# Kernel optimization log

Measured on AMD Instinct MI355X. Metric: run time of the kernel, lower is better.

The kernel has to match this reference:

```python
import jax, jax.numpy as jnp
import numpy as np

BIG = 1e9
EPS_BETA = 1e-6
EPS_BN = 1e-5

N_NODES = 50000
N_EDGES = 800000
IN_DIM = 128
OUT_DIM = 128


def setup_inputs() -> dict:
    key = jax.random.key(0)
    ks = jax.random.split(key, 8)
    h = jax.random.normal(ks[0], (N_NODES, IN_DIM), dtype=jnp.float32)
    src = jax.random.randint(ks[1], (N_EDGES,), 0, N_NODES, dtype=jnp.int32)
    dst = jax.random.randint(ks[2], (N_EDGES,), 0, N_NODES, dtype=jnp.int32)
    sigma_GD = jax.random.uniform(ks[3], (N_EDGES,), dtype=jnp.float32)
    fc_w = jax.random.normal(ks[4], (IN_DIM, OUT_DIM), dtype=jnp.float32) / np.sqrt(IN_DIM)
    fc_b = jax.random.normal(ks[5], (OUT_DIM,), dtype=jnp.float32) * 0.01
    attn_w = jax.random.normal(ks[6], (2 * OUT_DIM, 1), dtype=jnp.float32) / np.sqrt(2 * OUT_DIM)
    attn_b = jax.random.normal(ks[7], (1,), dtype=jnp.float32) * 0.01
    bn_gamma = jnp.ones((OUT_DIM,), dtype=jnp.float32)
    bn_beta = jnp.zeros((OUT_DIM,), dtype=jnp.float32)
    return {"h": h, "src": src, "dst": dst, "sigma_GD": sigma_GD,
            "fc_w": fc_w, "fc_b": fc_b, "attn_w": attn_w, "attn_b": attn_b,
            "bn_gamma": bn_gamma, "bn_beta": bn_beta}


def reference(h, src, dst, sigma_GD, fc_w, fc_b, attn_w, attn_b, bn_gamma, bn_beta):
    n = h.shape[0]
    # node projection
    z = h @ fc_w + fc_b                                   # [N, D]
    z = jnp.where(jnp.isinf(z), BIG, z)
    # per-edge attention logits: concat(src,dst) @ W == src@W1 + dst@W2 (avoid concat materialization)
    d = z.shape[1]
    w_src, w_dst = attn_w[:d], attn_w[d:]
    z_src = z[src]                                        # [E, D]
    a = z_src @ w_src + z[dst] @ w_dst + attn_b           # [E, 1]
    a = jnp.where(jnp.isinf(a), BIG, a)
    e = jax.nn.leaky_relu(a, negative_slope=0.01)[:, 0]   # [E]
    # segment softmax over incoming edges (mailbox softmax)
    m = jax.ops.segment_max(e, dst, num_segments=n)       # [N]
    ex = jnp.exp(e - m[dst])
    denom = jax.ops.segment_sum(ex, dst, num_segments=n)  # [N]
    alpha = ex / denom[dst]                               # [E]
    # beta: sigma_GD normalized per destination node
    bsum = jax.ops.segment_sum(sigma_GD, dst, num_segments=n)
    beta = sigma_GD / (bsum[dst] + EPS_BETA)              # [E]
    # weighted scatter-sum of source features
    h_new = jax.ops.segment_sum((alpha * beta)[:, None] * z_src, dst, num_segments=n)  # [N, D]
    h_new = jnp.where(jnp.isinf(h_new), BIG, h_new)
    # BatchNorm1d (training-mode batch stats, biased variance, as torch does)
    mu = h_new.mean(axis=0)
    var = ((h_new - mu) ** 2).mean(axis=0)
    h_bn = (h_new - mu) * jax.lax.rsqrt(var + EPS_BN) * bn_gamma + bn_beta
    return jax.nn.elu(h_bn)
```

## Files before the change

### kernel.cpp

```cpp
#include <hip/hip_runtime.h>
#include <hip/hip_fp16.h>
#include <math.h>

#define N_NODES 50000
#define N_EDGES 800000
#define BIGV 1000000000.0f
#define NBLK_SCAN 196
#define NBLK_GEMM 3125

typedef _Float16 half8 __attribute__((ext_vector_type(8)));
typedef float floatx4 __attribute__((ext_vector_type(4)));

__device__ __forceinline__ float clampinf(float x) { return isinf(x) ? BIGV : x; }

__global__ __launch_bounds__(256) void k_wcast(const float* __restrict__ W,
                                               __half* __restrict__ wt,
                                               int* __restrict__ cursor,
                                               float* __restrict__ bns)
{
    int idx = blockIdx.x * 256 + threadIdx.x;
    int n = idx >> 7, k = idx & 127;
    wt[idx] = __float2half(W[k * 128 + n]);
    for (int i = idx; i < N_NODES; i += 16384) cursor[i] = 0;
    if (idx < 256) bns[idx] = 0.f;
}

__global__ __launch_bounds__(256) void k_gemm(
    const float* __restrict__ h, const __half* __restrict__ wt,
    const float* __restrict__ bias, const float* __restrict__ attn_w,
    const int* __restrict__ dst, __half* __restrict__ zh,
    float* __restrict__ sv, float* __restrict__ tv,
    int* __restrict__ cursor, int* __restrict__ rank)
{
    __shared__ _Float16 hA[16][136];
    __shared__ float spart[4][16], tpart[4][16];

    const int tid = threadIdx.x;
    const int lane = tid & 63;
    const int wv = tid >> 6;
    const int l16 = lane & 15;
    const int oct = lane >> 4;
    const int n0 = wv << 5;
    const int node0 = blockIdx.x << 4;

    const int e = blockIdx.x * 256 + tid;
    const int d = dst[e];
    {
        const float4* h4 = (const float4*)(h + (size_t)node0 * 128);
        for (int i = tid; i < 512; i += 256) {
            int r = i >> 5, c4 = i & 31;
            float4 v = h4[i];
            union { __half2 h2[2]; uint2 u; } pk;
            pk.h2[0] = __floats2half2_rn(v.x, v.y);
            pk.h2[1] = __floats2half2_rn(v.z, v.w);
            *(uint2*)&hA[r][c4 << 2] = pk.u;
        }
    }
    rank[e] = atomicAdd(&cursor[d], 1);

    half8 bfrag[4][2];
    #pragma unroll
    for (int kk = 0; kk < 4; ++kk)
        #pragma unroll
        for (int t = 0; t < 2; ++t)
            bfrag[kk][t] = *(const half8*)(wt + (size_t)(n0 + t * 16 + l16) * 128
                                              + kk * 32 + oct * 8);

    const float bv0 = bias[n0 + l16],         bv1 = bias[n0 + 16 + l16];
    const float ws0 = attn_w[n0 + l16],       ws1 = attn_w[n0 + 16 + l16];
    const float wd0 = attn_w[128 + n0 + l16], wd1 = attn_w[128 + n0 + 16 + l16];

    __syncthreads();

    floatx4 acc0 = {0.f, 0.f, 0.f, 0.f};
    floatx4 acc1 = {0.f, 0.f, 0.f, 0.f};
    #pragma unroll
    for (int kk = 0; kk < 4; ++kk) {
        half8 a = *(const half8*)&hA[l16][(kk << 5) + (oct << 3)];
        acc0 = __builtin_amdgcn_mfma_f32_16x16x32_f16(a, bfrag[kk][0], acc0, 0, 0, 0);
        acc1 = __builtin_amdgcn_mfma_f32_16x16x32_f16(a, bfrag[kk][1], acc1, 0, 0, 0);
    }

    float s_acc[4], t_acc[4];
    #pragma unroll
    for (int r = 0; r < 4; ++r) {
        float z0 = clampinf(acc0[r] + bv0);
        float z1 = clampinf(acc1[r] + bv1);
        const int row = (oct << 2) + r;
        zh[(size_t)(node0 + row) * 128 + n0 + l16]      = __float2half(z0);
        zh[(size_t)(node0 + row) * 128 + n0 + 16 + l16] = __float2half(z1);
        s_acc[r] = z0 * ws0 + z1 * ws1;
        t_acc[r] = z0 * wd0 + z1 * wd1;
    }
    #pragma unroll
    for (int r = 0; r < 4; ++r) {
        #pragma unroll
        for (int o = 1; o < 16; o <<= 1) {
            s_acc[r] += __shfl_xor(s_acc[r], o);
            t_acc[r] += __shfl_xor(t_acc[r], o);
        }
    }
    if (l16 == 0) {
        #pragma unroll
        for (int r = 0; r < 4; ++r) {
            spart[wv][(oct << 2) + r] = s_acc[r];
            tpart[wv][(oct << 2) + r] = t_acc[r];
        }
    }
    __syncthreads();
    if (tid < 16) {
        sv[node0 + tid] = spart[0][tid] + spart[1][tid] + spart[2][tid] + spart[3][tid];
        tv[node0 + tid] = tpart[0][tid] + tpart[1][tid] + tpart[2][tid] + tpart[3][tid];
    }
}

__global__ __launch_bounds__(256) void k_scan_bsum(const int* __restrict__ cursor,
                                                   int* __restrict__ bsum)
{
    __shared__ int s[256];
    const int t = threadIdx.x;
    const int idx = blockIdx.x * 256 + t;
    s[t] = (idx < N_NODES) ? cursor[idx] : 0;
    __syncthreads();
    for (int off = 128; off; off >>= 1) {
        if (t < off) s[t] += s[t + off];
        __syncthreads();
    }
    if (t == 0) bsum[blockIdx.x] = s[0];
}

__global__ __launch_bounds__(256) void k_scan_final(const int* __restrict__ bsum,
                                                    const int* __restrict__ cursor_in,
                                                    int* __restrict__ colptr)
{
    __shared__ int rs[256];
    __shared__ int s[256];
    const int t = threadIdx.x;

    int rv = (t < NBLK_SCAN) ? bsum[t] : 0;
    rs[t] = rv;
    __syncthreads();
    for (int off = 1; off < 256; off <<= 1) {
        int u = (t >= off) ? rs[t - off] : 0;
        __syncthreads();
        rs[t] += u;
        __syncthreads();
    }
    const int broot = (blockIdx.x > 0) ? rs[blockIdx.x - 1] : 0;
    if (blockIdx.x == 0 && t == 255) colptr[N_NODES] = rs[255];

    const int idx = blockIdx.x * 256 + t;
    int v = (idx < N_NODES) ? cursor_in[idx] : 0;
    s[t] = v;
    __syncthreads();
    for (int off = 1; off < 256; off <<= 1) {
        int u = (t >= off) ? s[t - off] : 0;
        __syncthreads();
        s[t] += u;
        __syncthreads();
    }
    if (idx < N_NODES) colptr[idx] = broot + s[t] - v;
}

__global__ void k_scatter(const int* __restrict__ src, const int* __restrict__ dst,
                          const float* __restrict__ sigma,
                          const int* __restrict__ rank, const int* __restrict__ colptr,
                          const float* __restrict__ sv, const float* __restrict__ tv,
                          const float* __restrict__ attn_b,
                          float4* __restrict__ recs)
{
    int e = blockIdx.x * 256 + threadIdx.x;
    if (e < N_EDGES) {
        int s = src[e];
        int d = dst[e];
        float a = sv[s] + tv[d] + attn_b[0];
        a = clampinf(a);
        float ev = a > 0.f ? a : 0.01f * a;
        int pos = colptr[d] + rank[e];
        float4 rec;
        rec.x = __int_as_float(s);
        rec.y = sigma[e];
        rec.z = ev;
        rec.w = 0.f;
        recs[pos] = rec;
    }
}

__global__ __launch_bounds__(256) void k_agg(
    const int* __restrict__ colptr, const float4* __restrict__ recs,
    const __half* __restrict__ zh, float* __restrict__ out)
{
    const int lane = threadIdx.x & 63;
    const int node = blockIdx.x * 4 + (threadIdx.x >> 6);
    if (node >= N_NODES) return;
    const int base = colptr[node];
    const int deg = colptr[node + 1] - base;

    const int grp = lane >> 4;
    const int l16 = lane & 15;
    float acc[8] = {0.f, 0.f, 0.f, 0.f, 0.f, 0.f, 0.f, 0.f};

    if (deg > 0) {
        if (deg <= 64) {
            int sidx = 0; float sig = 0.f, e = -INFINITY;
            if (lane < deg) {
                float4 r = recs[base + lane];
                sidx = __float_as_int(r.x); sig = r.y; e = r.z;
            }
            float m = e;
            for (int o = 32; o; o >>= 1) m = fmaxf(m, __shfl_xor(m, o));
            float p = (lane < deg) ? __expf(e - m) : 0.f;
            float dn = p, bs = sig;
            for (int o = 32; o; o >>= 1) {
                dn += __shfl_xor(dn, o);
                bs += __shfl_xor(bs, o);
            }
            const float coef = p * sig * (1.0f / dn) / (bs + 1e-6f);
            for (int c = 0; c < deg; c += 4) {
                const int j = c + grp;
                const int js = (j < deg) ? j : 0;
                float cf = __shfl(coef, js);
                int sj = __shfl(sidx, js);
                if (j < deg) {
                    uint4 raw = *(const uint4*)(zh + ((size_t)sj << 7) + (l16 << 3));
                    const __half2* hp = (const __half2*)&raw;
                    #pragma unroll
                    for (int k = 0; k < 4; ++k) {
                        float2 f = __half22float2(hp[k]);
                        acc[2*k]   = fmaf(cf, f.x, acc[2*k]);
                        acc[2*k+1] = fmaf(cf, f.y, acc[2*k+1]);
                    }
                }
            }
        } else {
            float m = -INFINITY;
            for (int i = lane; i < deg; i += 64) m = fmaxf(m, recs[base + i].z);
            for (int o = 32; o; o >>= 1) m = fmaxf(m, __shfl_xor(m, o));
            float dn = 0.f, bs = 0.f;
            for (int i = lane; i < deg; i += 64) {
                float4 r = recs[base + i];
                dn += __expf(r.z - m); bs += r.y;
            }
            for (int o = 32; o; o >>= 1) {
                dn += __shfl_xor(dn, o);
                bs += __shfl_xor(bs, o);
            }
            const float scale = (1.0f / dn) / (bs + 1e-6f);
            for (int c = 0; c < deg; c += 64) {
                int i = c + lane;
                int sidx = 0; float coef = 0.f;
                if (i < deg) {
                    float4 r = recs[base + i];
                    sidx = __float_as_int(r.x);
                    coef = __expf(r.z - m) * r.y * scale;
                }
                const int cnt = min(64, deg - c);
                for (int j = 0; j < cnt; j += 4) {
                    const int jj = j + grp;
                    const int js = (jj < cnt) ? jj : 0;
                    float cf = __shfl(coef, js);
                    int sj = __shfl(sidx, js);
                    if (jj < cnt) {
                        uint4 raw = *(const uint4*)(zh + ((size_t)sj << 7) + (l16 << 3));
                        const __half2* hp = (const __half2*)&raw;
                        #pragma unroll
                        for (int k = 0; k < 4; ++k) {
                            float2 f = __half22float2(hp[k]);
                            acc[2*k]   = fmaf(cf, f.x, acc[2*k]);
                            acc[2*k+1] = fmaf(cf, f.y, acc[2*k+1]);
                        }
                    }
                }
            }
        }
    }
    #pragma unroll
    for (int k = 0; k < 8; ++k) {
        acc[k] += __shfl_xor(acc[k], 16);
        acc[k] += __shfl_xor(acc[k], 32);
    }
    if (grp == 0) {
        float4 o0, o1;
        o0.x = clampinf(acc[0]); o0.y = clampinf(acc[1]);
        o0.z = clampinf(acc[2]); o0.w = clampinf(acc[3]);
        o1.x = clampinf(acc[4]); o1.y = clampinf(acc[5]);
        o1.z = clampinf(acc[6]); o1.w = clampinf(acc[7]);
        float4* op = (float4*)(out + (size_t)node * 128 + (l16 << 3));
        op[0] = o0; op[1] = o1;
    }
}

__global__ __launch_bounds__(256) void k_bnstats(const float* __restrict__ hnew,
                                                 float* __restrict__ sums)
{
    const int f = threadIdx.x & 127;
    const int half_ = threadIdx.x >> 7;
    float s = 0.f, q = 0.f;
    for (int node = blockIdx.x * 2 + half_; node < N_NODES; node += gridDim.x * 2) {
        float v = hnew[(size_t)node * 128 + f];
        s += v;
        q += v * v;
    }
    __shared__ float ls[256], lq[256];
    ls[threadIdx.x] = s; lq[threadIdx.x] = q;
    __syncthreads();
    if (half_ == 0) {
        s += ls[threadIdx.x + 128];
        q += lq[threadIdx.x + 128];
        atomicAdd(&sums[f], s);
        atomicAdd(&sums[128 + f], q);
    }
}

__global__ __launch_bounds__(256) void k_bnapply(float* __restrict__ io,
                                                 const float* __restrict__ sums,
                                                 const float* __restrict__ gamma,
                                                 const float* __restrict__ beta)
{
    const size_t idx = (size_t)blockIdx.x * 256 + threadIdx.x;
    const int f = (int)(idx & 127);
    const float invn = 1.0f / (float)N_NODES;
    float mu = sums[f] * invn;
    float var = fmaxf(sums[128 + f] * invn - mu * mu, 0.f);
    float rs = rsqrtf(var + 1e-5f);
    float x = io[idx];
    float y = (x - mu) * rs * gamma[f] + beta[f];
    io[idx] = y > 0.f ? y : expm1f(y);
}

extern "C" void kernel_launch(void* const* d_in, const int* in_sizes, int n_in,
                              void* d_out, int out_size, void* d_ws, size_t ws_size,
                              hipStream_t stream)
{
    const float* h      = (const float*)d_in[0];
    const int*   src    = (const int*)  d_in[1];
    const int*   dst    = (const int*)  d_in[2];
    const float* sigma  = (const float*)d_in[3];
    const float* fc_w   = (const float*)d_in[4];
    const float* fc_b   = (const float*)d_in[5];
    const float* attn_w = (const float*)d_in[6];
    const float* attn_b = (const float*)d_in[7];
    const float* gamma  = (const float*)d_in[8];
    const float* beta   = (const float*)d_in[9];
    float* out = (float*)d_out;

    float4* recs   = (float4*)d_ws;
    __half* zh     = (__half*)(recs + N_EDGES);
    float*  sv     = (float*)(zh + (size_t)N_NODES * 128);
    float*  tv     = sv + N_NODES;
    float*  bns    = tv + N_NODES;
    int*    colptr = (int*)(bns + 256);
    int*    cursor = colptr + 50004;
    int*    bsum   = cursor + N_NODES;
    int*    broot  = bsum + 256;
    __half* wt     = (__half*)(broot + 256);
    int*    rank   = (int*)(wt + 128 * 128);

    k_wcast     <<<64, 256, 0, stream>>>(fc_w, wt, cursor, bns);
    k_gemm      <<<NBLK_GEMM, 256, 0, stream>>>(h, wt, fc_b, attn_w, dst,
                                                zh, sv, tv, cursor, rank);
    k_scan_bsum <<<NBLK_SCAN, 256, 0, stream>>>(cursor, bsum);
    k_scan_final<<<NBLK_SCAN, 256, 0, stream>>>(bsum, cursor, colptr);
    k_scatter   <<<N_EDGES / 256, 256, 0, stream>>>(src, dst, sigma, rank, colptr,
                                                    sv, tv, attn_b, recs);
    k_agg       <<<N_NODES / 4, 256, 0, stream>>>(colptr, recs, zh, out);
    k_bnstats   <<<256, 256, 0, stream>>>(out, bns);
    k_bnapply   <<<(N_NODES * 128) / 256, 256, 0, stream>>>(out, bns, gamma, beta);
}
```

Measured before the change: 235.4 us.

## Vectorize batchnorm kernels and defer rank atomic past LDS-only barriers in GEMM

```diff
diff --git a/kernel.cpp b/kernel.cpp
--- a/kernel.cpp
+++ b/kernel.cpp
@@ -12,6 +12,13 @@
 typedef float floatx4 __attribute__((ext_vector_type(4)));
 
 __device__ __forceinline__ float clampinf(float x) { return isinf(x) ? BIGV : x; }
+
+__device__ __forceinline__ void barrier_lgkm_only() {
+    __builtin_amdgcn_sched_barrier(0);
+    asm volatile("s_waitcnt lgkmcnt(0)" ::: "memory");
+    __builtin_amdgcn_s_barrier();
+    __builtin_amdgcn_sched_barrier(0);
+}
 
 __global__ __launch_bounds__(256) void k_wcast(const float* __restrict__ W,
                                                __half* __restrict__ wt,
@@ -45,6 +52,7 @@
 
     const int e = blockIdx.x * 256 + tid;
     const int d = dst[e];
+
     {
         const float4* h4 = (const float4*)(h + (size_t)node0 * 128);
         for (int i = tid; i < 512; i += 256) {
@@ -56,7 +64,6 @@
             *(uint2*)&hA[r][c4 << 2] = pk.u;
         }
     }
-    rank[e] = atomicAdd(&cursor[d], 1);
 
     half8 bfrag[4][2];
     #pragma unroll
@@ -70,7 +77,10 @@
     const float ws0 = attn_w[n0 + l16],       ws1 = attn_w[n0 + 16 + l16];
     const float wd0 = attn_w[128 + n0 + l16], wd1 = attn_w[128 + n0 + 16 + l16];
 
-    __syncthreads();
+    __builtin_amdgcn_sched_barrier(0);
+    const int rk = atomicAdd(&cursor[d], 1);
+
+    barrier_lgkm_only();
 
     floatx4 acc0 = {0.f, 0.f, 0.f, 0.f};
     floatx4 acc1 = {0.f, 0.f, 0.f, 0.f};
@@ -107,11 +117,12 @@
             tpart[wv][(oct << 2) + r] = t_acc[r];
         }
     }
-    __syncthreads();
+    barrier_lgkm_only();
     if (tid < 16) {
         sv[node0 + tid] = spart[0][tid] + spart[1][tid] + spart[2][tid] + spart[3][tid];
         tv[node0 + tid] = tpart[0][tid] + tpart[1][tid] + tpart[2][tid] + tpart[3][tid];
     }
+    rank[e] = rk;
 }
 
 __global__ __launch_bounds__(256) void k_scan_bsum(const int* __restrict__ cursor,
@@ -293,22 +304,36 @@
 __global__ __launch_bounds__(256) void k_bnstats(const float* __restrict__ hnew,
                                                  float* __restrict__ sums)
 {
-    const int f = threadIdx.x & 127;
-    const int half_ = threadIdx.x >> 7;
-    float s = 0.f, q = 0.f;
-    for (int node = blockIdx.x * 2 + half_; node < N_NODES; node += gridDim.x * 2) {
-        float v = hnew[(size_t)node * 128 + f];
-        s += v;
-        q += v * v;
-    }
-    __shared__ float ls[256], lq[256];
-    ls[threadIdx.x] = s; lq[threadIdx.x] = q;
+    const int tid = threadIdx.x;
+    const int f4 = (tid & 31) << 2;
+    const int rgrp = tid >> 5;
+    float4 s = {0.f, 0.f, 0.f, 0.f}, q = {0.f, 0.f, 0.f, 0.f};
+    for (int node = blockIdx.x * 8 + rgrp; node < N_NODES; node += 256 * 8) {
+        float4 v = *(const float4*)(hnew + (size_t)node * 128 + f4);
+        s.x += v.x; s.y += v.y; s.z += v.z; s.w += v.w;
+        q.x += v.x * v.x; q.y += v.y * v.y; q.z += v.z * v.z; q.w += v.w * v.w;
+    }
+    __shared__ float4 ls[256], lq[256];
+    ls[tid] = s; lq[tid] = q;
     __syncthreads();
-    if (half_ == 0) {
-        s += ls[threadIdx.x + 128];
-        q += lq[threadIdx.x + 128];
-        atomicAdd(&sums[f], s);
-        atomicAdd(&sums[128 + f], q);
+    for (int off = 128; off >= 32; off >>= 1) {
+        if (tid < off) {
+            float4 a = ls[tid + off], b = lq[tid + off];
+            ls[tid].x += a.x; ls[tid].y += a.y; ls[tid].z += a.z; ls[tid].w += a.w;
+            lq[tid].x += b.x; lq[tid].y += b.y; lq[tid].z += b.z; lq[tid].w += b.w;
+        }
+        __syncthreads();
+    }
+    if (tid < 32) {
+        float4 fs = ls[tid], fq = lq[tid];
+        atomicAdd(&sums[f4 + 0], fs.x);
+        atomicAdd(&sums[f4 + 1], fs.y);
+        atomicAdd(&sums[f4 + 2], fs.z);
+        atomicAdd(&sums[f4 + 3], fs.w);
+        atomicAdd(&sums[128 + f4 + 0], fq.x);
+        atomicAdd(&sums[128 + f4 + 1], fq.y);
+        atomicAdd(&sums[128 + f4 + 2], fq.z);
+        atomicAdd(&sums[128 + f4 + 3], fq.w);
     }
 }
 
@@ -317,15 +342,30 @@
                                                  const float* __restrict__ gamma,
                                                  const float* __restrict__ beta)
 {
-    const size_t idx = (size_t)blockIdx.x * 256 + threadIdx.x;
-    const int f = (int)(idx & 127);
-    const float invn = 1.0f / (float)N_NODES;
-    float mu = sums[f] * invn;
-    float var = fmaxf(sums[128 + f] * invn - mu * mu, 0.f);
-    float rs = rsqrtf(var + 1e-5f);
-    float x = io[idx];
-    float y = (x - mu) * rs * gamma[f] + beta[f];
-    io[idx] = y > 0.f ? y : expm1f(y);
+    __shared__ float sc[128], sh[128];
+    const int tid = threadIdx.x;
+    if (tid < 128) {
+        const float invn = 1.0f / (float)N_NODES;
+        float mu = sums[tid] * invn;
+        float var = fmaxf(sums[128 + tid] * invn - mu * mu, 0.f);
+        float g = gamma[tid] * rsqrtf(var + 1e-5f);
+        sc[tid] = g;
+        sh[tid] = beta[tid] - mu * g;
+    }
+    __syncthreads();
+    const size_t idx = (size_t)blockIdx.x * 256 + tid;
+    const int f4 = ((int)idx & 31) << 2;
+    float4 x = ((const float4*)io)[idx];
+    float y0 = x.x * sc[f4 + 0] + sh[f4 + 0];
+    float y1 = x.y * sc[f4 + 1] + sh[f4 + 1];
+    float y2 = x.z * sc[f4 + 2] + sh[f4 + 2];
+    float y3 = x.w * sc[f4 + 3] + sh[f4 + 3];
+    float4 o;
+    o.x = y0 > 0.f ? y0 : expm1f(y0);
+    o.y = y1 > 0.f ? y1 : expm1f(y1);
+    o.z = y2 > 0.f ? y2 : expm1f(y2);
+    o.w = y3 > 0.f ? y3 : expm1f(y3);
+    ((float4*)io)[idx] = o;
 }
 
 extern "C" void kernel_launch(void* const* d_in, const int* in_sizes, int n_in,
@@ -365,5 +405,5 @@
                                                     sv, tv, attn_b, recs);
     k_agg       <<<N_NODES / 4, 256, 0, stream>>>(colptr, recs, zh, out);
     k_bnstats   <<<256, 256, 0, stream>>>(out, bns);
-    k_bnapply   <<<(N_NODES * 128) / 256, 256, 0, stream>>>(out, bns, gamma, beta);
-}
+    k_bnapply   <<<(N_NODES * 128) / (256 * 4), 256, 0, stream>>>(out, bns, gamma, beta);
+}
```

Result: no change. 231.4 us (-1.7%).
